# Performance work log

Measured on AMD Instinct MI355X. Metric: run time of the kernel, lower is better.

The kernel has to match this reference:

```python
import jax, jax.numpy as jnp
import numpy as np

D = 128
N_COLS = 64
EPS = 1e-6
# op MLP index per feature token: mult, add, cos, absdiff, sub_ab, sub_ba, div_ab, div_ba
MLP_IDX = np.array([0, 1, 2, 3, 4, 4, 5, 5])


def setup_inputs() -> dict:
    key = jax.random.key(0)
    ks = jax.random.split(key, 16)
    B = 64
    pairs = np.array([(i, j) for i in range(N_COLS) for j in range(i + 1, N_COLS)], dtype=np.int32)
    P = pairs.shape[0]  # 2016
    s = 0.02
    inp = {
        "x": jax.random.normal(ks[0], (B, N_COLS, D), dtype=jnp.float32),
        "presence": jax.random.randint(ks[1], (B, N_COLS), 0, 2, dtype=jnp.int32),
        "idx_i": jnp.asarray(pairs[:, 0]),
        "idx_j": jnp.asarray(pairs[:, 1]),
        # 6 op MLPs (multiply, add, cosine, abs_diff, subtract, divide): d -> d/2 -> d
        "ops_W1": jax.random.normal(ks[2], (6, D, D // 2), dtype=jnp.float32) * s,
        "ops_b1": jnp.zeros((6, D // 2), dtype=jnp.float32),
        "ops_W2": jax.random.normal(ks[3], (6, D // 2, D), dtype=jnp.float32) * s,
        "ops_b2": jnp.zeros((6, D), dtype=jnp.float32),
        # presence MLP: 4 -> d/2 -> d
        "pres_W1": jax.random.normal(ks[4], (4, D // 2), dtype=jnp.float32) * s,
        "pres_b1": jnp.zeros((D // 2,), dtype=jnp.float32),
        "pres_W2": jax.random.normal(ks[5], (D // 2, D), dtype=jnp.float32) * s,
        "pres_b2": jnp.zeros((D,), dtype=jnp.float32),
        # fusion MLP: 9d -> 2d -> d
        "fus_W1": jax.random.normal(ks[6], (9 * D, 2 * D), dtype=jnp.float32) * s,
        "fus_b1": jnp.zeros((2 * D,), dtype=jnp.float32),
        "fus_W2": jax.random.normal(ks[7], (2 * D, D), dtype=jnp.float32) * s,
        "fus_b2": jnp.zeros((D,), dtype=jnp.float32),
    }
    return inp


def reference(x, presence, idx_i, idx_j,
              ops_W1, ops_b1, ops_W2, ops_b2,
              pres_W1, pres_b1, pres_W2, pres_b2,
              fus_W1, fus_b1, fus_W2, fus_b2):
    B = x.shape[0]
    P = idx_i.shape[0]
    A = x[:, idx_i]  # [B, P, D]
    Bv = x[:, idx_j]  # [B, P, D]
    An = A / (jnp.linalg.norm(A, axis=-1, keepdims=True) + EPS)
    Bn = Bv / (jnp.linalg.norm(Bv, axis=-1, keepdims=True) + EPS)
    # 8 elementwise relation features [8, B, P, D]
    feats = jnp.stack([
        A * Bv,                 # multiply
        A + Bv,                 # add
        An * Bn,                # cosine (elementwise normalized product)
        jnp.abs(A - Bv),        # abs diff
        A - Bv,                 # subtract A->B
        Bv - A,                 # subtract B->A
        A / (Bv + EPS),         # divide A/B
        Bv / (A + EPS),         # divide B/A
    ])
    W1 = ops_W1[MLP_IDX]  # [8, D, D/2]
    b1 = ops_b1[MLP_IDX]
    W2 = ops_W2[MLP_IDX]
    b2 = ops_b2[MLP_IDX]
    h = jax.nn.relu(jnp.einsum('kbpd,kdh->kbph', feats, W1) + b1[:, None, None, :])
    tok = jnp.einsum('kbph,khd->kbpd', h, W2) + b2[:, None, None, :]  # [8, B, P, D]
    # presence flags [B, P, 4]
    pa = presence[:, idx_i].astype(x.dtype)
    pb = presence[:, idx_j].astype(x.dtype)
    flags = jnp.stack([pa * pb, pa * (1 - pb), (1 - pa) * pb, (1 - pa) * (1 - pb)], axis=-1)
    ptok = jax.nn.relu(flags @ pres_W1 + pres_b1) @ pres_W2 + pres_b2  # [B, P, D]
    # concat 9 tokens -> fusion MLP -> 1 token per pair
    cat = jnp.concatenate([jnp.transpose(tok, (1, 2, 0, 3)).reshape(B, P, 8 * D), ptok], axis=-1)
    out = jax.nn.relu(cat @ fus_W1 + fus_b1) @ fus_W2 + fus_b2  # [B, P, D]
    return out
```

## Files before the change

### kernel.cpp

```cpp
#include <hip/hip_runtime.h>

#define EPS 1e-6f

using bfrag = __attribute__((ext_vector_type(8))) short;
using hfrag = __attribute__((ext_vector_type(8))) _Float16;
using ffrag = __attribute__((ext_vector_type(4))) float;
typedef unsigned short ushortT;

#define MFMA(a, b, c) __builtin_amdgcn_mfma_f32_16x16x32_bf16((a), (b), (c), 0, 0, 0)
#define MFMA16(a, b, c) __builtin_amdgcn_mfma_f32_16x16x32_f16((a), (b), (c), 0, 0, 0)

__device__ __forceinline__ ushortT bf_hi(float x) {
  unsigned u = __builtin_bit_cast(unsigned, x);
  return (ushortT)((u + 0x7FFFu + ((u >> 16) & 1u)) >> 16);
}
__device__ __forceinline__ float uaf(unsigned u) { return __builtin_bit_cast(float, u); }
__device__ __forceinline__ unsigned cvtpk(float a, float b) {
  unsigned d;
  asm("v_cvt_pk_bf16_f32 %0, %1, %2" : "=v"(d) : "v"(a), "v"(b));
  return d;
}
__device__ __forceinline__ unsigned pkf16(float a, float b) {
  unsigned d;
  asm("v_cvt_pkrtz_f16_f32 %0, %1, %2" : "=v"(d) : "v"(a), "v"(b));
  return d;
}
__device__ __forceinline__ int op_of(int k) { return (k < 4) ? k : ((k >> 1) + 2); }

__global__ void prologue(const float* __restrict__ ops_W1,
                         const float* __restrict__ ops_W2,
                         const float* __restrict__ ops_b2,
                         const float* __restrict__ pres_W1,
                         const float* __restrict__ pres_b1,
                         const float* __restrict__ pres_W2,
                         const float* __restrict__ pres_b2,
                         const float* __restrict__ fus_W1,
                         const float* __restrict__ fus_b1,
                         const float* __restrict__ fus_W2,
                         ushortT* __restrict__ Gp,
                         ushortT* __restrict__ W1p,
                         ushortT* __restrict__ W2p,
                         float* __restrict__ cb) {
  const int blk = blockIdx.x;
  const int tid = threadIdx.x;

  if (blk < 512) {
    int r = blk, n = tid;
    int slot = r >> 6;
    const int KMAP[8] = {0, 2, 3, 4, 1, 5, 6, 7};
    int k = KMAP[slot];
    int op = op_of(k);
    const float* w2 = ops_W2 + (size_t)(op * 64 + (r & 63)) * 128;
    const float* w1 = fus_W1 + (size_t)(k * 128) * 256 + n;
    float a0 = 0.f, a1 = 0.f, a2 = 0.f, a3 = 0.f;
#pragma unroll 8
    for (int d = 0; d < 128; d += 4) {
      a0 = fmaf(w2[d], w1[(size_t)d * 256], a0);
      a1 = fmaf(w2[d + 1], w1[(size_t)(d + 1) * 256], a1);
      a2 = fmaf(w2[d + 2], w1[(size_t)(d + 2) * 256], a2);
      a3 = fmaf(w2[d + 3], w1[(size_t)(d + 3) * 256], a3);
    }
    float acc = (a0 + a1) + (a2 + a3);
    ushortT outv;
    if (slot < 6) {
      _Float16 hv = (_Float16)acc;
      outv = __builtin_bit_cast(ushortT, hv);
    } else {
      outv = bf_hi(acc);
    }
    int nt = n >> 4, kk = r >> 5, quad = (r >> 3) & 3, j = r & 7;
    int lane = quad * 16 + (n & 15);
    Gp[((nt * 16 + kk) * 64 + lane) * 8 + j] = outv;
  } else if (blk < 544) {
    int gid = (blk - 512) * 256 + tid;
    int lane = gid & 63, kk = (gid >> 6) & 3, nt = (gid >> 8) & 3, k = gid >> 10;
    int op = op_of(k);
    int col = nt * 16 + (lane & 15);
#pragma unroll
    for (int j = 0; j < 8; ++j) {
      int d = kk * 32 + ((lane >> 4) & 3) * 8 + j;
      float w = ops_W1[((size_t)op * 128 + d) * 64 + col];
      ushortT outv;
      if (k < 6) {
        _Float16 hv = (_Float16)w;
        outv = __builtin_bit_cast(ushortT, hv);
      } else {
        outv = bf_hi(w);
      }
      W1p[gid * 8 + j] = outv;
    }
  } else if (blk < 560) {
    int gid = (blk - 544) * 256 + tid;
    int lane = gid & 63, kk = (gid >> 6) & 7, nt = gid >> 9;
    int col = nt * 16 + (lane & 15);
#pragma unroll
    for (int j = 0; j < 8; ++j) {
      int d = kk * 32 + ((lane >> 4) & 3) * 8 + j;
      W2p[gid * 8 + j] = bf_hi(fus_W2[(size_t)d * 128 + col]);
    }
  } else {
    int c = blk - 560, n = tid;
    __shared__ float hrelu[64];
    __shared__ float ptok[128];
    if (n < 64) hrelu[n] = fmaxf(pres_W1[c * 64 + n] + pres_b1[n], 0.f);
    __syncthreads();
    if (n < 128) {
      float p0 = pres_b2[n], p1 = 0.f;
#pragma unroll 8
      for (int hh = 0; hh < 64; hh += 2) {
        p0 = fmaf(hrelu[hh], pres_W2[hh * 128 + n], p0);
        p1 = fmaf(hrelu[hh + 1], pres_W2[(hh + 1) * 128 + n], p1);
      }
      ptok[n] = p0 + p1;
    }
    __syncthreads();
    float acc = fus_b1[n];
#pragma unroll 4
    for (int d = 0; d < 128; ++d)
      acc = fmaf(ptok[d], fus_W1[(size_t)(1024 + d) * 256 + n], acc);
    float acc2 = 0.f;
    for (int k = 0; k < 8; ++k) {
      int op = op_of(k);
#pragma unroll 4
      for (int d = 0; d < 128; ++d)
        acc2 = fmaf(ops_b2[op * 128 + d], fus_W1[(size_t)(k * 128 + d) * 256 + n], acc2);
    }
    cb[c * 256 + n] = acc + acc2;
  }
}

#define XS_ROWS 40

struct Frag2 {
  bfrag h[4];
  bfrag l[4];
};

union U4 {
  unsigned u[4];
  bfrag b;
};

#define FM_MUL 0
#define FM_ADD 1
#define FM_SUB 2
#define FM_ABS 3
#define FM_DAB 4
#define FM_DBA 5

template <int M>
__device__ __forceinline__ void buildFragsF16S(const float* RA, const float* RB, int quad,
                                               bfrag (&h)[4]) {
#pragma unroll
  for (int kk = 0; kk < 4; ++kk) {
    float4 a0 = *(const float4*)(RA + kk * 32 + quad * 8);
    float4 a1 = *(const float4*)(RA + kk * 32 + quad * 8 + 4);
    float4 b0 = *(const float4*)(RB + kk * 32 + quad * 8);
    float4 b1 = *(const float4*)(RB + kk * 32 + quad * 8 + 4);
    float a[8] = {a0.x, a0.y, a0.z, a0.w, a1.x, a1.y, a1.z, a1.w};
    float b[8] = {b0.x, b0.y, b0.z, b0.w, b1.x, b1.y, b1.z, b1.w};
    U4 uh;
#pragma unroll
    for (int p = 0; p < 4; ++p) {
      float f0, f1;
      if constexpr (M == FM_MUL)      { f0 = a[2*p] * b[2*p]; f1 = a[2*p+1] * b[2*p+1]; }
      else if constexpr (M == FM_ADD) { f0 = a[2*p] + b[2*p]; f1 = a[2*p+1] + b[2*p+1]; }
      else if constexpr (M == FM_SUB) { f0 = a[2*p] - b[2*p]; f1 = a[2*p+1] - b[2*p+1]; }
      else                            { f0 = fabsf(a[2*p] - b[2*p]); f1 = fabsf(a[2*p+1] - b[2*p+1]); }
      uh.u[p] = pkf16(f0, f1);
    }
    h[kk] = uh.b;
  }
}

template <int M>
__device__ __forceinline__ void buildFragsS(const float* RA, const float* RB, int quad,
                                            Frag2& fr) {
#pragma unroll
  for (int kk = 0; kk < 4; ++kk) {
    float4 a0 = *(const float4*)(RA + kk * 32 + quad * 8);
    float4 a1 = *(const float4*)(RA + kk * 32 + quad * 8 + 4);
    float4 b0 = *(const float4*)(RB + kk * 32 + quad * 8);
    float4 b1 = *(const float4*)(RB + kk * 32 + quad * 8 + 4);
    float a[8] = {a0.x, a0.y, a0.z, a0.w, a1.x, a1.y, a1.z, a1.w};
    float b[8] = {b0.x, b0.y, b0.z, b0.w, b1.x, b1.y, b1.z, b1.w};
    U4 uh, ul;
#pragma unroll
    for (int p = 0; p < 4; ++p) {
      float f0, f1;
      if constexpr (M == FM_DAB) {
        f0 = a[2*p] * __builtin_amdgcn_rcpf(b[2*p] + EPS);
        f1 = a[2*p+1] * __builtin_amdgcn_rcpf(b[2*p+1] + EPS);
      } else {
        f0 = b[2*p] * __builtin_amdgcn_rcpf(a[2*p] + EPS);
        f1 = b[2*p+1] * __builtin_amdgcn_rcpf(a[2*p+1] + EPS);
      }
      unsigned dh = cvtpk(f0, f1);
      float r0 = f0 - uaf(dh << 16);
      float r1 = f1 - uaf(dh & 0xFFFF0000u);
      uh.u[p] = dh;
      ul.u[p] = cvtpk(r0, r1);
    }
    fr.h[kk] = uh.b;
    fr.l[kk] = ul.b;
  }
}

__device__ __forceinline__ void normPass(const float* RA, const float* RB, int quad,
                                         float& sa, float& sb) {
  sa = 0.f; sb = 0.f;
#pragma unroll
  for (int kk = 0; kk < 4; ++kk) {
    float4 a0 = *(const float4*)(RA + kk * 32 + quad * 8);
    float4 a1 = *(const float4*)(RA + kk * 32 + quad * 8 + 4);
    float4 b0 = *(const float4*)(RB + kk * 32 + quad * 8);
    float4 b1 = *(const float4*)(RB + kk * 32 + quad * 8 + 4);
    sa = fmaf(a0.x, a0.x, sa); sa = fmaf(a0.y, a0.y, sa);
    sa = fmaf(a0.z, a0.z, sa); sa = fmaf(a0.w, a0.w, sa);
    sa = fmaf(a1.x, a1.x, sa); sa = fmaf(a1.y, a1.y, sa);
    sa = fmaf(a1.z, a1.z, sa); sa = fmaf(a1.w, a1.w, sa);
    sb = fmaf(b0.x, b0.x, sb); sb = fmaf(b0.y, b0.y, sb);
    sb = fmaf(b0.z, b0.z, sb); sb = fmaf(b0.w, b0.w, sb);
    sb = fmaf(b1.x, b1.x, sb); sb = fmaf(b1.y, b1.y, sb);
    sb = fmaf(b1.z, b1.z, sb); sb = fmaf(b1.w, b1.w, sb);
  }
}

template <int K>
__device__ __forceinline__ void mmAllF16(const bfrag (&h)[4], int lane,
                                         const ushortT* __restrict__ W1p, ffrag (&s)[4]) {
#pragma unroll
  for (int nt = 0; nt < 4; ++nt) {
    const ushortT* wp = W1p + ((K * 4 + nt) * 4) * 512 + lane * 8;
    ffrag acc = {0.f, 0.f, 0.f, 0.f};
#pragma unroll
    for (int kk = 0; kk < 4; ++kk) {
      hfrag w = __builtin_bit_cast(hfrag, *(const bfrag*)(wp + kk * 512));
      acc = MFMA16(__builtin_bit_cast(hfrag, h[kk]), w, acc);
    }
    s[nt] = acc;
  }
}

template <int K>
__device__ __forceinline__ void mmAll(const Frag2& fr, int lane,
                                      const ushortT* __restrict__ W1p, ffrag (&s)[4]) {
#pragma unroll
  for (int nt = 0; nt < 4; ++nt) {
    const ushortT* wp = W1p + ((K * 4 + nt) * 4) * 512 + lane * 8;
    ffrag acc = {0.f, 0.f, 0.f, 0.f};
#pragma unroll
    for (int kk = 0; kk < 4; ++kk) {
      bfrag w = *(const bfrag*)(wp + kk * 512);
      acc = MFMA(fr.h[kk], w, acc);
      acc = MFMA(fr.l[kk], w, acc);
    }
    s[nt] = acc;
  }
}

__device__ __forceinline__ void ldBias(const float* __restrict__ ops_b1, int OP, int c0,
                                       float (&bb)[4]) {
#pragma unroll
  for (int nt = 0; nt < 4; ++nt) bb[nt] = ops_b1[OP * 64 + nt * 16 + c0];
}

__device__ __forceinline__ void storeHf(ffrag s, float scl, float bias, int rbase, int col,
                                        ushortT (*Hh)[136]) {
  float v[4];
#pragma unroll
  for (int i = 0; i < 4; ++i) v[i] = fmaxf(fmaf(s[i], scl, bias), 0.f);
#pragma unroll
  for (int p = 0; p < 2; ++p) {
    unsigned d = pkf16(v[2 * p], v[2 * p + 1]);
    Hh[rbase + 2 * p][col] = (ushortT)(d & 0xFFFFu);
    Hh[rbase + 2 * p + 1][col] = (ushortT)(d >> 16);
  }
}

__device__ __forceinline__ void storeHf4(const ffrag (&s)[4], float scl, const float (&bb)[4],
                                         int rbase, int colbase, int c0,
                                         ushortT (*Hh)[136]) {
#pragma unroll
  for (int nt = 0; nt < 4; ++nt)
    storeHf(s[nt], scl, bb[nt], rbase, colbase + nt * 16 + c0, Hh);
}

__device__ __forceinline__ void storeH(ffrag s, float bias, int rbase, int col,
                                       ushortT (*Hh)[136], ushortT (*Hl)[136]) {
  float v[4];
#pragma unroll
  for (int i = 0; i < 4; ++i) v[i] = fmaxf(s[i] + bias, 0.f);
#pragma unroll
  for (int p = 0; p < 2; ++p) {
    unsigned dh = cvtpk(v[2 * p], v[2 * p + 1]);
    float r0 = v[2 * p] - uaf(dh << 16);
    float r1 = v[2 * p + 1] - uaf(dh & 0xFFFF0000u);
    unsigned dl = cvtpk(r0, r1);
    Hh[rbase + 2 * p][col] = (ushortT)(dh & 0xFFFFu);
    Hh[rbase + 2 * p + 1][col] = (ushortT)(dh >> 16);
    Hl[rbase + 2 * p][col] = (ushortT)(dl & 0xFFFFu);
    Hl[rbase + 2 * p + 1][col] = (ushortT)(dl >> 16);
  }
}

__device__ __forceinline__ void storeH4(const ffrag (&s)[4], const float (&bb)[4],
                                        int rbase, int colbase, int c0,
                                        ushortT (*Hh)[136], ushortT (*Hl)[136]) {
#pragma unroll
  for (int nt = 0; nt < 4; ++nt)
    storeH(s[nt], bb[nt], rbase, colbase + nt * 16 + c0, Hh, Hl);
}

__device__ __forceinline__ void p3roundF16(int r, int wv, int lane, int quad, int c0,
                                           ushortT (*Hh)[136],
                                           const ushortT* __restrict__ Gp,
                                           ffrag (&u)[4], ffrag (&v)[4]) {
#pragma unroll
  for (int kk = 0; kk < 4; ++kk) {
    hfrag ah0 = __builtin_bit_cast(hfrag, *(const bfrag*)&Hh[c0][kk * 32 + quad * 8]);
    hfrag ah1 = __builtin_bit_cast(hfrag, *(const bfrag*)&Hh[16 + c0][kk * 32 + quad * 8]);
#pragma unroll
    for (int nt4 = 0; nt4 < 4; ++nt4) {
      hfrag g = __builtin_bit_cast(
          hfrag, *(const bfrag*)(Gp + (((wv * 4 + nt4) * 16 + r * 4 + kk) * 64 + lane) * 8));
      u[nt4] = MFMA16(ah0, g, u[nt4]);
      v[nt4] = MFMA16(ah1, g, v[nt4]);
    }
  }
}

__device__ __forceinline__ void p3round(int r, int wv, int lane, int quad, int c0,
                                        ushortT (*Hh)[136], ushortT (*Hl)[136],
                                        const ushortT* __restrict__ Gp,
                                        ffrag (&u)[4], ffrag (&v)[4]) {
#pragma unroll
  for (int kk = 0; kk < 4; ++kk) {
    bfrag ah0 = *(const bfrag*)&Hh[c0][kk * 32 + quad * 8];
    bfrag al0 = *(const bfrag*)&Hl[c0][kk * 32 + quad * 8];
    bfrag ah1 = *(const bfrag*)&Hh[16 + c0][kk * 32 + quad * 8];
    bfrag al1 = *(const bfrag*)&Hl[16 + c0][kk * 32 + quad * 8];
#pragma unroll
    for (int nt4 = 0; nt4 < 4; ++nt4) {
      bfrag g = *(const bfrag*)(Gp + (((wv * 4 + nt4) * 16 + r * 4 + kk) * 64 + lane) * 8);
      u[nt4] = MFMA(ah0, g, u[nt4]);
      u[nt4] = MFMA(al0, g, u[nt4]);
      v[nt4] = MFMA(ah1, g, v[nt4]);
      v[nt4] = MFMA(al1, g, v[nt4]);
    }
  }
}

__global__ __launch_bounds__(256, 4)
void drel_main(const float* __restrict__ x, const int* __restrict__ presence,
               const int* __restrict__ idx_i, const int* __restrict__ idx_j,
               const float* __restrict__ ops_b1, const float* __restrict__ fus_b2,
               const ushortT* __restrict__ W1p, const ushortT* __restrict__ Gp,
               const ushortT* __restrict__ W2p, const float* __restrict__ cbias,
               float* __restrict__ out) {
  __shared__ __align__(16) char smem[30464];
  float   (*Xs)[132]  = reinterpret_cast<float(*)[132]>(smem);
  ushortT (*Hl)[136]  = reinterpret_cast<ushortT(*)[136]>(smem);
  ushortT (*Dh)[264]  = reinterpret_cast<ushortT(*)[264]>(smem);
  ushortT (*Hh)[136]  = reinterpret_cast<ushortT(*)[136]>(smem + 21120);
  int* sCombo = reinterpret_cast<int*>(smem + 29824);
  unsigned* maskW = reinterpret_cast<unsigned*>(smem + 29952);
  int* rowLocal = reinterpret_cast<int*>(smem + 29960);
  int* rowOf = reinterpret_cast<int*>(smem + 30216);

  const int tid = threadIdx.x;
  const int wv = tid >> 6, lane = tid & 63, quad = lane >> 4, c0 = lane & 15;
  const int wtile = wv & 1;
  const int wrole = wv >> 1;

  const int blk = blockIdx.x;
  const int b = blk / 63;
  const int p0 = (blk % 63) * 32;

  if (tid < 2) maskW[tid] = 0;
  __syncthreads();
  if (tid < 32) {
    int p = p0 + tid;
    int ri = idx_i[p], rj = idx_j[p];
    int pa = presence[b * 64 + ri];
    int pb = presence[b * 64 + rj];
    sCombo[tid] = pa ? (pb ? 0 : 1) : (pb ? 2 : 3);
    atomicOr(&maskW[ri >> 5], 1u << (ri & 31));
    atomicOr(&maskW[rj >> 5], 1u << (rj & 31));
  }
  __syncthreads();
  const unsigned long long mask =
      ((unsigned long long)maskW[1] << 32) | (unsigned long long)maskW[0];
  const int nrows = __popcll(mask);
  if (tid < 64 && ((mask >> tid) & 1)) {
    int slot = __popcll(mask & ((1ull << tid) - 1ull));
    rowLocal[tid] = slot;
    rowOf[slot] = tid;
  }
  __syncthreads();

  const float* xb = x + (size_t)b * 64 * 128;
  for (int s = tid; s < nrows * 32; s += 256) {
    int row = s >> 5, c4 = (s & 31) * 4;
    *(float4*)&Xs[row][c4] = *(const float4*)(xb + (size_t)rowOf[row] * 128 + c4);
  }

  const int rI = rowLocal[idx_i[p0 + wtile * 16 + c0]];
  const int rJ = rowLocal[idx_j[p0 + wtile * 16 + c0]];
  const int rbase = wtile * 16 + quad * 4;

  ffrag u[4], v[4];
  {
    int comb0[4], comb1[4];
#pragma unroll
    for (int i = 0; i < 4; ++i) {
      comb0[i] = sCombo[quad * 4 + i];
      comb1[i] = sCombo[16 + quad * 4 + i];
    }
#pragma unroll
    for (int nt4 = 0; nt4 < 4; ++nt4) {
      int col = (wv * 4 + nt4) * 16 + c0;
#pragma unroll
      for (int i = 0; i < 4; ++i) {
        u[nt4][i] = cbias[comb0[i] * 256 + col];
        v[nt4][i] = cbias[comb1[i] * 256 + col];
      }
    }
  }
  __syncthreads();

  const float* RA = Xs[rI];
  const float* RB = Xs[rJ];
  bfrag fh[4];
  ffrag s4[4];

  {
    buildFragsF16S<FM_MUL>(RA, RB, quad, fh);
    ffrag s[4];
    float bb[4];
    if (wrole == 0) {
      ldBias(ops_b1, 0, c0, bb);
      mmAllF16<0>(fh, lane, W1p, s);
      storeHf4(s, 1.f, bb, rbase, 0, c0, Hh);
    } else {
      float sa, sb;
      normPass(RA, RB, quad, sa, sb);
      sa += __shfl_xor(sa, 16); sb += __shfl_xor(sb, 16);
      sa += __shfl_xor(sa, 32); sb += __shfl_xor(sb, 32);
      float scl = (1.f / (sqrtf(sa) + EPS)) * (1.f / (sqrtf(sb) + EPS));
      ldBias(ops_b1, 2, c0, bb);
      mmAllF16<2>(fh, lane, W1p, s);
      storeHf4(s, scl, bb, rbase, 64, c0, Hh);
    }
  }
  __syncthreads();
  p3roundF16(0, wv, lane, quad, c0, Hh, Gp, u, v);
  __syncthreads();

  {
    float bb[4];
    if (wrole == 0) {
      buildFragsF16S<FM_ABS>(RA, RB, quad, fh);
      ffrag s[4];
      ldBias(ops_b1, 3, c0, bb);
      mmAllF16<3>(fh, lane, W1p, s);
      storeHf4(s, 1.f, bb, rbase, 0, c0, Hh);
    } else {
      buildFragsF16S<FM_SUB>(RA, RB, quad, fh);
      ldBias(ops_b1, 4, c0, bb);
      mmAllF16<4>(fh, lane, W1p, s4);
      storeHf4(s4, 1.f, bb, rbase, 64, c0, Hh);
    }
  }
  __syncthreads();
  p3roundF16(1, wv, lane, quad, c0, Hh, Gp, u, v);
  __syncthreads();

  {
    float bb[4];
    if (wrole == 0) {
      buildFragsF16S<FM_ADD>(RA, RB, quad, fh);
      ffrag s[4];
      ldBias(ops_b1, 1, c0, bb);
      mmAllF16<1>(fh, lane, W1p, s);
      storeHf4(s, 1.f, bb, rbase, 0, c0, Hh);
    } else {
      ldBias(ops_b1, 4, c0, bb);
      storeHf4(s4, -1.f, bb, rbase, 64, c0, Hh);
    }
  }
  __syncthreads();
  p3roundF16(2, wv, lane, quad, c0, Hh, Gp, u, v);
  __syncthreads();

  {
    Frag2 fr;
    if (wrole == 0) buildFragsS<FM_DAB>(RA, RB, quad, fr);
    else            buildFragsS<FM_DBA>(RA, RB, quad, fr);
    __syncthreads();
    ffrag s[4];
    float bb[4];
    ldBias(ops_b1, 5, c0, bb);
    if (wrole == 0) {
      mmAll<6>(fr, lane, W1p, s);
      storeH4(s, bb, rbase, 0, c0, Hh, Hl);
    } else {
      mmAll<7>(fr, lane, W1p, s);
      storeH4(s, bb, rbase, 64, c0, Hh, Hl);
    }
  }
  __syncthreads();
  p3round(3, wv, lane, quad, c0, Hh, Hl, Gp, u, v);
  __syncthreads();

#pragma unroll
  for (int nt4 = 0; nt4 < 4; ++nt4) {
    int col = (wv * 4 + nt4) * 16 + c0;
#pragma unroll
    for (int p = 0; p < 2; ++p) {
      unsigned du = cvtpk(fmaxf(u[nt4][2 * p], 0.f), fmaxf(u[nt4][2 * p + 1], 0.f));
      Dh[quad * 4 + 2 * p][col] = (ushortT)(du & 0xFFFFu);
      Dh[quad * 4 + 2 * p + 1][col] = (ushortT)(du >> 16);
      unsigned dv = cvtpk(fmaxf(v[nt4][2 * p], 0.f), fmaxf(v[nt4][2 * p + 1], 0.f));
      Dh[16 + quad * 4 + 2 * p][col] = (ushortT)(dv & 0xFFFFu);
      Dh[16 + quad * 4 + 2 * p + 1][col] = (ushortT)(dv >> 16);
    }
  }
  __syncthreads();

  ffrag o[2], q[2];
#pragma unroll
  for (int nt2 = 0; nt2 < 2; ++nt2) {
    float bias = fus_b2[(wv * 2 + nt2) * 16 + c0];
    o[nt2] = ffrag{bias, bias, bias, bias};
    q[nt2] = o[nt2];
  }
#pragma unroll
  for (int kk = 0; kk < 8; ++kk) {
    bfrag dh0 = *(const bfrag*)&Dh[c0][kk * 32 + quad * 8];
    bfrag dh1 = *(const bfrag*)&Dh[16 + c0][kk * 32 + quad * 8];
#pragma unroll
    for (int nt2 = 0; nt2 < 2; ++nt2) {
      bfrag w = *(const bfrag*)(W2p + (((wv * 2 + nt2) * 8 + kk) * 64 + lane) * 8);
      o[nt2] = MFMA(dh0, w, o[nt2]);
      q[nt2] = MFMA(dh1, w, q[nt2]);
    }
  }
#pragma unroll
  for (int nt2 = 0; nt2 < 2; ++nt2) {
    int col = (wv * 2 + nt2) * 16 + c0;
#pragma unroll
    for (int i = 0; i < 4; ++i) {
      int row = quad * 4 + i;
      out[(size_t)(b * 2016 + p0 + row) * 128 + col] = o[nt2][i];
      out[(size_t)(b * 2016 + p0 + 16 + row) * 128 + col] = q[nt2][i];
    }
  }
}

extern "C" void kernel_launch(void* const* d_in, const int* in_sizes, int n_in,
                              void* d_out, int out_size, void* d_ws, size_t ws_size,
                              hipStream_t stream) {
  const float* x        = (const float*)d_in[0];
  const int*   presence = (const int*)d_in[1];
  const int*   idx_i    = (const int*)d_in[2];
  const int*   idx_j    = (const int*)d_in[3];
  const float* ops_W1   = (const float*)d_in[4];
  const float* ops_b1   = (const float*)d_in[5];
  const float* ops_W2   = (const float*)d_in[6];
  const float* ops_b2   = (const float*)d_in[7];
  const float* pres_W1  = (const float*)d_in[8];
  const float* pres_b1  = (const float*)d_in[9];
  const float* pres_W2  = (const float*)d_in[10];
  const float* pres_b2  = (const float*)d_in[11];
  const float* fus_W1   = (const float*)d_in[12];
  const float* fus_b1   = (const float*)d_in[13];
  const float* fus_W2   = (const float*)d_in[14];
  const float* fus_b2   = (const float*)d_in[15];

  char* ws = (char*)d_ws;
  ushortT* Gp  = (ushortT*)(ws);
  ushortT* W1p = (ushortT*)(ws + 262144);
  ushortT* W2p = (ushortT*)(ws + 393216);
  float*   CB  = (float*)(ws + 458752);

  prologue<<<564, 256, 0, stream>>>(ops_W1, ops_W2, ops_b2, pres_W1, pres_b1,
                                    pres_W2, pres_b2, fus_W1, fus_b1, fus_W2,
                                    Gp, W1p, W2p, CB);
  drel_main<<<4032, 256, 0, stream>>>(x, presence, idx_i, idx_j, ops_b1, fus_b2,
                                      W1p, Gp, W2p, CB, (float*)d_out);
}
```

Baseline: 253.2 us.

## Double-buffer hidden-activation tile to overlap first-layer MLPs with fusion rounds

Splits the shared hidden buffer into two halves (HhA/HhB) so that each fusion-layer MFMA round reads one buffer while the next op-MLP pair writes the other. This removes about three block-wide barriers per block and lets independent matrix work interleave within a phase. In exchange the shared memory footprint grows and launch bounds drop from 4 to 3 blocks per CU, which may reduce occupancy or change register allocation.

```diff
diff --git a/kernel.cpp b/kernel.cpp
--- a/kernel.cpp
+++ b/kernel.cpp
@@ -129,8 +129,6 @@
   }
 }
 
-#define XS_ROWS 40
-
 struct Frag2 {
   bfrag h[4];
   bfrag l[4];
@@ -351,22 +349,23 @@
   }
 }
 
-__global__ __launch_bounds__(256, 4)
+__global__ __launch_bounds__(256, 3)
 void drel_main(const float* __restrict__ x, const int* __restrict__ presence,
                const int* __restrict__ idx_i, const int* __restrict__ idx_j,
                const float* __restrict__ ops_b1, const float* __restrict__ fus_b2,
                const ushortT* __restrict__ W1p, const ushortT* __restrict__ Gp,
                const ushortT* __restrict__ W2p, const float* __restrict__ cbias,
                float* __restrict__ out) {
-  __shared__ __align__(16) char smem[30464];
+  __shared__ __align__(16) char smem[39168];
   float   (*Xs)[132]  = reinterpret_cast<float(*)[132]>(smem);
   ushortT (*Hl)[136]  = reinterpret_cast<ushortT(*)[136]>(smem);
   ushortT (*Dh)[264]  = reinterpret_cast<ushortT(*)[264]>(smem);
-  ushortT (*Hh)[136]  = reinterpret_cast<ushortT(*)[136]>(smem + 21120);
-  int* sCombo = reinterpret_cast<int*>(smem + 29824);
-  unsigned* maskW = reinterpret_cast<unsigned*>(smem + 29952);
-  int* rowLocal = reinterpret_cast<int*>(smem + 29960);
-  int* rowOf = reinterpret_cast<int*>(smem + 30216);
+  ushortT (*HhA)[136] = reinterpret_cast<ushortT(*)[136]>(smem + 21120);
+  ushortT (*HhB)[136] = reinterpret_cast<ushortT(*)[136]>(smem + 29824);
+  int* sCombo = reinterpret_cast<int*>(smem + 38528);
+  unsigned* maskW = reinterpret_cast<unsigned*>(smem + 38656);
+  int* rowLocal = reinterpret_cast<int*>(smem + 38664);
+  int* rowOf = reinterpret_cast<int*>(smem + 38920);
 
   const int tid = threadIdx.x;
   const int wv = tid >> 6, lane = tid & 63, quad = lane >> 4, c0 = lane & 15;
@@ -441,7 +440,7 @@
     if (wrole == 0) {
       ldBias(ops_b1, 0, c0, bb);
       mmAllF16<0>(fh, lane, W1p, s);
-      storeHf4(s, 1.f, bb, rbase, 0, c0, Hh);
+      storeHf4(s, 1.f, bb, rbase, 0, c0, HhA);
     } else {
       float sa, sb;
       normPass(RA, RB, quad, sa, sb);
@@ -450,11 +449,9 @@
       float scl = (1.f / (sqrtf(sa) + EPS)) * (1.f / (sqrtf(sb) + EPS));
       ldBias(ops_b1, 2, c0, bb);
       mmAllF16<2>(fh, lane, W1p, s);
-      storeHf4(s, scl, bb, rbase, 64, c0, Hh);
-    }
-  }
-  __syncthreads();
-  p3roundF16(0, wv, lane, quad, c0, Hh, Gp, u, v);
+      storeHf4(s, scl, bb, rbase, 64, c0, HhA);
+    }
+  }
   __syncthreads();
 
   {
@@ -464,16 +461,15 @@
       ffrag s[4];
       ldBias(ops_b1, 3, c0, bb);
       mmAllF16<3>(fh, lane, W1p, s);
-      storeHf4(s, 1.f, bb, rbase, 0, c0, Hh);
+      storeHf4(s, 1.f, bb, rbase, 0, c0, HhB);
     } else {
       buildFragsF16S<FM_SUB>(RA, RB, quad, fh);
       ldBias(ops_b1, 4, c0, bb);
       mmAllF16<4>(fh, lane, W1p, s4);
-      storeHf4(s4, 1.f, bb, rbase, 64, c0, Hh);
-    }
-  }
-  __syncthreads();
-  p3roundF16(1, wv, lane, quad, c0, Hh, Gp, u, v);
+      storeHf4(s4, 1.f, bb, rbase, 64, c0, HhB);
+    }
+    p3roundF16(0, wv, lane, quad, c0, HhA, Gp, u, v);
+  }
   __syncthreads();
 
   {
@@ -483,34 +479,38 @@
       ffrag s[4];
       ldBias(ops_b1, 1, c0, bb);
       mmAllF16<1>(fh, lane, W1p, s);
-      storeHf4(s, 1.f, bb, rbase, 0, c0, Hh);
+      storeHf4(s, 1.f, bb, rbase, 0, c0, HhA);
     } else {
       ldBias(ops_b1, 4, c0, bb);
-      storeHf4(s4, -1.f, bb, rbase, 64, c0, Hh);
-    }
-  }
-  __syncthreads();
-  p3roundF16(2, wv, lane, quad, c0, Hh, Gp, u, v);
-  __syncthreads();
-
+      storeHf4(s4, -1.f, bb, rbase, 64, c0, HhA);
+    }
+    p3roundF16(1, wv, lane, quad, c0, HhB, Gp, u, v);
+  }
+  __syncthreads();
+
+  Frag2 fr3;
   {
-    Frag2 fr;
-    if (wrole == 0) buildFragsS<FM_DAB>(RA, RB, quad, fr);
-    else            buildFragsS<FM_DBA>(RA, RB, quad, fr);
-    __syncthreads();
+    if (wrole == 0) buildFragsS<FM_DAB>(RA, RB, quad, fr3);
+    else            buildFragsS<FM_DBA>(RA, RB, quad, fr3);
+    p3roundF16(2, wv, lane, quad, c0, HhA, Gp, u, v);
+  }
+  __syncthreads();
+
+  {
     ffrag s[4];
     float bb[4];
     ldBias(ops_b1, 5, c0, bb);
     if (wrole == 0) {
-      mmAll<6>(fr, lane, W1p, s);
-      storeH4(s, bb, rbase, 0, c0, Hh, Hl);
+      mmAll<6>(fr3, lane, W1p, s);
+      storeH4(s, bb, rbase, 0, c0, HhB, Hl);
     } else {
-      mmAll<7>(fr, lane, W1p, s);
-      storeH4(s, bb, rbase, 64, c0, Hh, Hl);
-    }
-  }
-  __syncthreads();
-  p3round(3, wv, lane, quad, c0, Hh, Hl, Gp, u, v);
+      mmAll<7>(fr3, lane, W1p, s);
+      storeH4(s, bb, rbase, 64, c0, HhB, Hl);
+    }
+  }
+  __syncthreads();
+
+  p3round(3, wv, lane, quad, c0, HhB, Hl, Gp, u, v);
   __syncthreads();
 
 #pragma unroll
```

Result: slower. 274.8 us (+8.5%).
